# Performance work log

Measured on AMD Instinct MI355X. Metric: run time of the kernel, lower is better.

Reference implementation:

```python
import jax, jax.numpy as jnp
import numpy as np

S, B, C = 7, 2, 20
L_COORD, L_NOOBJ = 5.0, 0.5
BATCH = 16384


def setup_inputs() -> dict:
    key = jax.random.key(0)
    k1, k2, k3 = jax.random.split(key, 3)
    pred = jax.random.normal(k1, (BATCH, S, S, 5 * B + C), dtype=jnp.float32)
    target = jax.random.uniform(k2, (BATCH, S, S, 5 * B + C), dtype=jnp.float32)
    conf = target[..., 4]
    target = target.at[..., 4].set(jnp.where(conf > 0.9, conf, 0.0))
    # per-cell branch choice (replaces python random.random() > 0.5 per object)
    choice = jax.random.randint(k3, (BATCH, S, S), 0, 2, dtype=jnp.int32)
    return {"pred": pred, "target": target, "choice": choice}


def reference(pred, target, choice):
    dt = pred.dtype
    tconf = target[..., 4]
    obj = tconf > 0                      # [B,S,S]
    m = obj.astype(dt)
    n_obj = jnp.maximum(m.sum(), 1.0)
    c = choice.astype(bool)              # True -> box 1, False -> box 2
    cE = c[..., None]

    pxy = jnp.where(cE, pred[..., 0:2], pred[..., 5:7])
    pwh = jnp.where(cE, pred[..., 2:4], pred[..., 7:9])
    txy = jnp.where(cE, target[..., 0:2], target[..., 5:7])
    twh = jnp.where(cE, target[..., 2:4], target[..., 7:9])
    twh = jnp.where(obj[..., None], twh, 1.0)  # sqrt-safe outside obj mask
    pobj = jnp.where(c, pred[..., 4], pred[..., 9])
    tobj = jnp.where(c, tconf, target[..., 9])

    # per-object: mean over 2 elems for xy and for (wh - sqrt(twh)), summed over objects
    loc_cell = ((pxy - txy) ** 2).mean(-1) + ((pwh - jnp.sqrt(twh)) ** 2).mean(-1)
    loc_loss = L_COORD * (m * loc_cell).sum()
    obj_loss = (m * (pobj - tobj) ** 2).sum()

    nm = (tconf == 0).astype(dt)
    n_no = jnp.maximum(nm.sum(), 1.0)
    noobj_loss = L_NOOBJ * (
        (nm * (pred[..., 4] - tconf) ** 2).sum() / n_no
        + (nm * (pred[..., 9] - target[..., 9]) ** 2).sum() / n_no
    )

    # faithful to original: softmax applied BEFORE CrossEntropyLoss (double softmax)
    logits = pred[..., 5 * B:5 * B + C]
    sm = jax.nn.softmax(logits, axis=-1)
    logp = jax.nn.log_softmax(sm, axis=-1)
    tcls = jnp.argmax(target[..., 5 * B:5 * B + C], axis=-1)
    ce = -jnp.take_along_axis(logp, tcls[..., None], axis=-1)[..., 0]
    cls_loss = (m * ce).sum() / n_obj

    return (loc_loss, cls_loss, obj_loss, noobj_loss)
```

## Files before the change

### kernel.cpp

```cpp
#include <hip/hip_runtime.h>
#include <math.h>


constexpr int NCH = 30;
constexpr int CC  = 20;
constexpr int PAD = 16;

__global__ __launch_bounds__(256) void yolo_main(
    const float* __restrict__ pred, const float* __restrict__ target,
    const int* __restrict__ choice, float* __restrict__ acc, int ncells)
{
    int cell = blockIdx.x * 256 + threadIdx.x;

    float s_loc = 0.f, s_ce = 0.f, s_obj = 0.f, s_no = 0.f;
    float n_obj = 0.f, n_no = 0.f;

    if (cell < ncells) {
        const float2* P2 = (const float2*)(pred + (size_t)cell * NCH);
        const float2* T2 = (const float2*)(target + (size_t)cell * NCH);
        float p[NCH], t[NCH];
        #pragma unroll
        for (int i = 0; i < NCH / 2; ++i) {
            float2 v = P2[i]; p[2 * i] = v.x; p[2 * i + 1] = v.y;
        }
        #pragma unroll
        for (int i = 0; i < NCH / 2; ++i) {
            float2 w = T2[i]; t[2 * i] = w.x; t[2 * i + 1] = w.y;
        }
        bool c = choice[cell] != 0;

        float tconf = t[4];
        bool  obj = tconf > 0.0f;
        float m = obj ? 1.0f : 0.0f;

        float pxy0 = c ? p[0] : p[5];
        float pxy1 = c ? p[1] : p[6];
        float pwh0 = c ? p[2] : p[7];
        float pwh1 = c ? p[3] : p[8];
        float pobj = c ? p[4] : p[9];
        float txy0 = c ? t[0] : t[5];
        float txy1 = c ? t[1] : t[6];
        float twh0 = c ? t[2] : t[7];
        float twh1 = c ? t[3] : t[8];
        if (!obj) { twh0 = 1.0f; twh1 = 1.0f; }
        float tobj = c ? tconf : t[9];

        float dx = pxy0 - txy0, dy = pxy1 - txy1;
        float dw = pwh0 - sqrtf(twh0), dh = pwh1 - sqrtf(twh1);
        float loc_cell = 0.5f * (dx * dx + dy * dy) + 0.5f * (dw * dw + dh * dh);
        s_loc = m * loc_cell;

        float dob = pobj - tobj;
        s_obj = m * dob * dob;

        float nm = (tconf == 0.0f) ? 1.0f : 0.0f;
        float d4 = p[4] - tconf, d9 = p[9] - t[9];
        s_no = nm * (d4 * d4 + d9 * d9);

        n_obj = m;
        n_no  = nm;

        int   tcls  = 0;
        float tbest = t[10];
        #pragma unroll
        for (int i = 1; i < CC; ++i) {
            float v = t[10 + i];
            if (v > tbest) { tbest = v; tcls = i; }
        }
        float mx = p[10];
        #pragma unroll
        for (int i = 1; i < CC; ++i) mx = fmaxf(mx, p[10 + i]);
        float e[CC];
        float Z = 0.f;
        #pragma unroll
        for (int i = 0; i < CC; ++i) { e[i] = __expf(p[10 + i] - mx); Z += e[i]; }
        float rZ = 1.0f / Z;
        float Z2 = 0.f, sm_t = 0.f;
        #pragma unroll
        for (int i = 0; i < CC; ++i) {
            float sm = e[i] * rZ;
            Z2 += __expf(sm);
            if (i == tcls) sm_t = sm;
        }
        float ce = __logf(Z2) - sm_t;
        s_ce = m * ce;
    }

    #pragma unroll
    for (int off = 32; off > 0; off >>= 1) {
        s_loc += __shfl_down(s_loc, off);
        s_ce  += __shfl_down(s_ce,  off);
        s_obj += __shfl_down(s_obj, off);
        s_no  += __shfl_down(s_no,  off);
        n_obj += __shfl_down(n_obj, off);
        n_no  += __shfl_down(n_no,  off);
    }

    __shared__ float red[4][6];
    int wave = threadIdx.x >> 6;
    int lane = threadIdx.x & 63;
    if (lane == 0) {
        red[wave][0] = s_loc; red[wave][1] = s_ce;  red[wave][2] = s_obj;
        red[wave][3] = s_no;  red[wave][4] = n_obj; red[wave][5] = n_no;
    }
    __syncthreads();
    if (threadIdx.x < 6) {
        float v = red[0][threadIdx.x] + red[1][threadIdx.x] +
                  red[2][threadIdx.x] + red[3][threadIdx.x];
        atomicAdd(&acc[threadIdx.x * PAD], v);
    }
}

__global__ void yolo_final(const float* __restrict__ acc, float* __restrict__ out) {
    float S_loc = acc[0 * PAD], S_ce = acc[1 * PAD], S_obj = acc[2 * PAD];
    float S_no  = acc[3 * PAD], N_ob = acc[4 * PAD], N_no = acc[5 * PAD];
    out[0] = 5.0f * S_loc;
    out[1] = S_ce / fmaxf(N_ob, 1.0f);
    out[2] = S_obj;
    out[3] = 0.5f * S_no / fmaxf(N_no, 1.0f);
}

extern "C" void kernel_launch(void* const* d_in, const int* in_sizes, int n_in,
                              void* d_out, int out_size, void* d_ws, size_t ws_size,
                              hipStream_t stream) {
    const float* pred   = (const float*)d_in[0];
    const float* target = (const float*)d_in[1];
    const int*   choice = (const int*)d_in[2];
    float* out = (float*)d_out;
    float* acc = (float*)d_ws;

    int ncells = in_sizes[2];
    hipMemsetAsync(d_ws, 0, 6 * PAD * sizeof(float), stream);
    int blocks = (ncells + 255) / 256;
    yolo_main<<<blocks, 256, 0, stream>>>(pred, target, choice, acc, ncells);
    yolo_final<<<1, 1, 0, stream>>>(acc, out);
}
```

Measured before the change: 232.6 us.

## Stage cell data through shared memory with coalesced float4 loads

Each block now loads its 128 cells of pred and target into LDS using fully coalesced float4 loads, then every thread reads its own 30-float cell from shared memory. Before, each thread did strided float2 global loads at a 120-byte stride. Block size drops from 256 to 128 threads to keep the LDS footprint at about 30KB per block. The cost is an extra barrier, LDS bank conflicts from the stride-30 reads, and possibly lower occupancy from the LDS use.

```diff
diff --git a/kernel.cpp b/kernel.cpp
--- a/kernel.cpp
+++ b/kernel.cpp
@@ -5,29 +5,54 @@
 constexpr int NCH = 30;
 constexpr int CC  = 20;
 constexpr int PAD = 16;
+constexpr int T   = 128;
+constexpr int CPB = 128;
+constexpr int NV  = CPB * NCH / 4;
 
-__global__ __launch_bounds__(256) void yolo_main(
+__global__ __launch_bounds__(T) void yolo_main(
     const float* __restrict__ pred, const float* __restrict__ target,
     const int* __restrict__ choice, float* __restrict__ acc, int ncells)
 {
-    int cell = blockIdx.x * 256 + threadIdx.x;
+    __shared__ float sbuf[2 * CPB * NCH];
+    const int tid = threadIdx.x;
+    const long long cell0 = (long long)blockIdx.x * CPB;
+    const int remain = ncells - (int)cell0;
+
+    if (remain >= CPB) {
+        const float4* Pg = (const float4*)(pred + cell0 * NCH);
+        const float4* Tg = (const float4*)(target + cell0 * NCH);
+        #pragma unroll
+        for (int j = 0; j < 2 * NV / T; ++j) {
+            int k = j * T + tid;
+            float4 v;
+            if (k < NV) v = Pg[k]; else v = Tg[k - NV];
+            *(float4*)&sbuf[k * 4] = v;
+        }
+    } else {
+        int nf = remain * NCH;
+        for (int idx = tid; idx < nf; idx += T) {
+            sbuf[idx]             = pred[cell0 * NCH + idx];
+            sbuf[CPB * NCH + idx] = target[cell0 * NCH + idx];
+        }
+    }
+    __syncthreads();
 
     float s_loc = 0.f, s_ce = 0.f, s_obj = 0.f, s_no = 0.f;
     float n_obj = 0.f, n_no = 0.f;
 
-    if (cell < ncells) {
-        const float2* P2 = (const float2*)(pred + (size_t)cell * NCH);
-        const float2* T2 = (const float2*)(target + (size_t)cell * NCH);
+    if (cell0 + tid < ncells) {
+        const float* sp  = &sbuf[tid * NCH];
+        const float* stt = &sbuf[CPB * NCH + tid * NCH];
         float p[NCH], t[NCH];
         #pragma unroll
         for (int i = 0; i < NCH / 2; ++i) {
-            float2 v = P2[i]; p[2 * i] = v.x; p[2 * i + 1] = v.y;
+            float2 v = *(const float2*)&sp[2 * i];  p[2*i] = v.x; p[2*i+1] = v.y;
         }
         #pragma unroll
         for (int i = 0; i < NCH / 2; ++i) {
-            float2 w = T2[i]; t[2 * i] = w.x; t[2 * i + 1] = w.y;
+            float2 w = *(const float2*)&stt[2 * i]; t[2*i] = w.x; t[2*i+1] = w.y;
         }
-        bool c = choice[cell] != 0;
+        bool c = choice[cell0 + tid] != 0;
 
         float tconf = t[4];
         bool  obj = tconf > 0.0f;
@@ -47,8 +72,7 @@
 
         float dx = pxy0 - txy0, dy = pxy1 - txy1;
         float dw = pwh0 - sqrtf(twh0), dh = pwh1 - sqrtf(twh1);
-        float loc_cell = 0.5f * (dx * dx + dy * dy) + 0.5f * (dw * dw + dh * dh);
-        s_loc = m * loc_cell;
+        s_loc = m * (0.5f * (dx * dx + dy * dy) + 0.5f * (dw * dw + dh * dh));
 
         float dob = pobj - tobj;
         s_obj = m * dob * dob;
@@ -82,8 +106,7 @@
             Z2 += __expf(sm);
             if (i == tcls) sm_t = sm;
         }
-        float ce = __logf(Z2) - sm_t;
-        s_ce = m * ce;
+        s_ce = m * (__logf(Z2) - sm_t);
     }
 
     #pragma unroll
@@ -96,18 +119,17 @@
         n_no  += __shfl_down(n_no,  off);
     }
 
-    __shared__ float red[4][6];
-    int wave = threadIdx.x >> 6;
-    int lane = threadIdx.x & 63;
+    __shared__ float red[2][6];
+    int wave = tid >> 6;
+    int lane = tid & 63;
     if (lane == 0) {
         red[wave][0] = s_loc; red[wave][1] = s_ce;  red[wave][2] = s_obj;
         red[wave][3] = s_no;  red[wave][4] = n_obj; red[wave][5] = n_no;
     }
     __syncthreads();
-    if (threadIdx.x < 6) {
-        float v = red[0][threadIdx.x] + red[1][threadIdx.x] +
-                  red[2][threadIdx.x] + red[3][threadIdx.x];
-        atomicAdd(&acc[threadIdx.x * PAD], v);
+    if (tid < 6) {
+        float v = red[0][tid] + red[1][tid];
+        atomicAdd(&acc[tid * PAD], v);
     }
 }
 
@@ -131,7 +153,7 @@
 
     int ncells = in_sizes[2];
     hipMemsetAsync(d_ws, 0, 6 * PAD * sizeof(float), stream);
-    int blocks = (ncells + 255) / 256;
-    yolo_main<<<blocks, 256, 0, stream>>>(pred, target, choice, acc, ncells);
+    int blocks = (ncells + CPB - 1) / CPB;
+    yolo_main<<<blocks, T, 0, stream>>>(pred, target, choice, acc, ncells);
     yolo_final<<<1, 1, 0, stream>>>(acc, out);
 }
```

New measurement: 303.7 us. 1.31x slower.
